# Performance work log

Measured on AMD Instinct MI355X. Metric: run time of the kernel, lower is better.

## Reference

```python
import jax, jax.numpy as jnp
import numpy as np

B, D, T = 32, 1024, 1000
LMAX = 200
VOCAB = 80
BLANK = VOCAB - 1
NEG = -1e30


def setup_inputs() -> dict:
    key = jax.random.key(0)
    ks = jax.random.split(key, 8)
    decoder_outputs = jax.random.normal(ks[0], (B, D, T), dtype=jnp.float32)
    target_text = jax.random.randint(ks[1], (B, LMAX), 0, BLANK, dtype=jnp.int32)
    decoder_lengths = jax.random.randint(ks[2], (B,), T // 2, T + 1, dtype=jnp.int32)
    target_lengths = jax.random.randint(ks[3], (B,), 1, LMAX + 1, dtype=jnp.int32)
    # learned params (dropout is identity in eval / deterministic reference)
    W1 = jax.random.normal(ks[4], (D, D), dtype=jnp.float32) * (1.0 / np.sqrt(D))
    b1 = jnp.zeros((D,), dtype=jnp.float32)
    W2 = jax.random.normal(ks[5], (D, VOCAB), dtype=jnp.float32) * (1.0 / np.sqrt(D))
    b2 = jnp.zeros((VOCAB,), dtype=jnp.float32)
    return {"decoder_outputs": decoder_outputs, "target_text": target_text,
            "decoder_lengths": decoder_lengths, "target_lengths": target_lengths,
            "W1": W1, "b1": b1, "W2": W2, "b2": b2}


def _ctc_nll(log_probs, targets, input_lengths, target_lengths):
    # log_probs: [T, B, V]; standard CTC alpha (forward) DP over extended labels.
    Tt, Bb, V = log_probs.shape
    L = targets.shape[1]
    S = 2 * L + 1
    ext = jnp.full((Bb, S), BLANK, dtype=targets.dtype).at[:, 1::2].set(targets)
    ext_m2 = jnp.pad(ext, ((0, 0), (2, 0)), constant_values=BLANK)[:, :S]
    allow_skip = (ext != BLANK) & (ext != ext_m2)
    allow_skip = allow_skip.at[:, :2].set(False)

    lp0 = log_probs[0]  # [B, V]
    alpha0 = jnp.full((Bb, S), NEG, dtype=log_probs.dtype)
    alpha0 = alpha0.at[:, 0].set(lp0[:, BLANK])
    alpha0 = alpha0.at[:, 1].set(jnp.take_along_axis(lp0, targets[:, :1], axis=1)[:, 0])

    def step(alpha, inp):
        lp_t, t = inp
        emit = jnp.take_along_axis(lp_t, ext, axis=1)  # [B, S]
        a2 = jnp.pad(alpha, ((0, 0), (1, 0)), constant_values=NEG)[:, :S]
        a3 = jnp.pad(alpha, ((0, 0), (2, 0)), constant_values=NEG)[:, :S]
        a3 = jnp.where(allow_skip, a3, NEG)
        new = jnp.logaddexp(jnp.logaddexp(alpha, a2), a3) + emit
        alpha = jnp.where((t < input_lengths)[:, None], new, alpha)
        return alpha, None

    alpha, _ = jax.lax.scan(step, alpha0, (log_probs[1:], jnp.arange(1, Tt)))
    i1 = (2 * target_lengths - 1)[:, None]
    i2 = (2 * target_lengths)[:, None]
    last = jnp.logaddexp(jnp.take_along_axis(alpha, i1, axis=1)[:, 0],
                         jnp.take_along_axis(alpha, i2, axis=1)[:, 0])
    nll = -last
    # zero_infinity=True: invalid alignments -> 0 loss
    return jnp.where(last > NEG / 2, nll, 0.0)


def reference(decoder_outputs, target_text, decoder_lengths, target_lengths, W1, b1, W2, b2):
    x = jnp.transpose(decoder_outputs, (0, 2, 1))          # [B, T, D]
    h = jax.nn.relu(jnp.einsum('btd,de->bte', x, W1) + b1)  # proj + ReLU (dropout=identity)
    logits = jnp.einsum('btd,dv->btv', h, W2) + b2          # [B, T, V]
    log_probs = jax.nn.log_softmax(logits, axis=2)
    log_probs = jnp.transpose(log_probs, (1, 0, 2))         # [T, B, V]
    ctc_loss = _ctc_nll(log_probs, target_text, decoder_lengths, target_lengths)
    return (ctc_loss / decoder_lengths.astype(jnp.float32)).mean()
```

## Files before the change

### kernel.cpp

```cpp
#include <hip/hip_runtime.h>
#include <cstdint>
#include <cstddef>

#define BN_ 32
#define DD_ 1024
#define TT_ 1000
#define LMAX_ 200
#define VC_ 80
#define BLANK_ 79
#define SS_ 401
#define SPAD 512
#define EMW 320
#define NEGV (-1e30f)

typedef _Float16 half8 __attribute__((ext_vector_type(8)));
typedef _Float16 half4 __attribute__((ext_vector_type(4)));
typedef float f32x4 __attribute__((ext_vector_type(4)));

__device__ __forceinline__ void async16(const void* g, void* l) {
  __builtin_amdgcn_global_load_lds(
      (const __attribute__((address_space(1))) unsigned int*)g,
      (__attribute__((address_space(3))) unsigned int*)l, 16, 0, 0);
}

__global__ __launch_bounds__(512) void transpose_all_kernel(
    const float* __restrict__ dec, const float* __restrict__ W1,
    const float* __restrict__ W2, _Float16* __restrict__ Af,
    _Float16* __restrict__ W1T, _Float16* __restrict__ W2T) {
  __shared__ _Float16 T2[64 * 256];
  int z = blockIdx.z;
  const float* in; _Float16* out; int C;
  const int R = 1024;
  if (z < 32) {
    in = dec + (size_t)z * R * TT_;
    out = Af + (size_t)z * TT_ * R;
    C = TT_;
  } else if (z == 32) {
    in = W1; out = W1T; C = 1024;
  } else {
    in = W2; out = W2T; C = VC_;
  }
  int c0 = blockIdx.x * 256, r0 = blockIdx.y * 64;
  if (c0 >= C) return;
  int tid = threadIdx.x;
  int cl = tid & 63, w = tid >> 6;
  int cch = c0 + 4 * cl;
  bool cv = (cch < C);
#pragma unroll
  for (int i = 0; i < 8; ++i) {
    int rl = w * 8 + i;
    f32x4 f = {0.f, 0.f, 0.f, 0.f};
    if (cv) f = *(const f32x4*)(in + (size_t)(r0 + rl) * C + cch);
    half4 hv = {(_Float16)f.x, (_Float16)f.y, (_Float16)f.z, (_Float16)f.w};
    *(half4*)&T2[rl * 256 + 4 * cl] = hv;
  }
  __syncthreads();
  {
    int cr = tid & 255, rh = (tid >> 8) * 32;
    if (c0 + cr < C) {
      half8 ho[4];
#pragma unroll
      for (int k = 0; k < 4; ++k)
#pragma unroll
        for (int j = 0; j < 8; ++j)
          ho[k][j] = T2[(rh + k * 8 + j) * 256 + cr];
      _Float16* op = out + (size_t)(c0 + cr) * R + r0 + rh;
#pragma unroll
      for (int k = 0; k < 4; ++k) *(half8*)&op[k * 8] = ho[k];
    }
  }
}

__device__ __forceinline__ void stage_half(const _Float16* __restrict__ X,
                                           int x0, int kt, int h,
                                           _Float16* lds, int tid, int K) {
#pragma unroll
  for (int jj = 0; jj < 2; ++jj) {
    int seg = tid + 512 * jj;
    int row = seg >> 3, slot = seg & 7;
    int cg = slot ^ (row & 7);
    async16(X + (size_t)(x0 + h * 128 + row) * K + kt * 64 + cg * 8,
            lds + seg * 8);
  }
}

__global__ __launch_bounds__(512, 2) void gemm_relu_kernel(
    const _Float16* __restrict__ A, const _Float16* __restrict__ Bt,
    const float* __restrict__ bias, _Float16* __restrict__ H,
    int M, int N, int K) {
  __shared__ __align__(16) _Float16 sA[2][16384];
  __shared__ __align__(16) _Float16 sB[2][16384];
  int tid = threadIdx.x;
  int wave = tid >> 6, lane = tid & 63;
  int quad = lane >> 4, r16 = lane & 15;
  int wm = wave >> 2, wn = wave & 3;

  int orig = blockIdx.x, nwg = gridDim.x;
  int xcd = orig & 7, loc = orig >> 3;
  int qq = nwg >> 3, rr = nwg & 7;
  int wg = (xcd < rr ? xcd * (qq + 1) : rr * (qq + 1) + (xcd - rr) * qq) + loc;
  int m0 = (wg >> 2) * 256, n0 = (wg & 3) * 256;

  f32x4 acc[4][8];
#pragma unroll
  for (int q = 0; q < 4; ++q)
#pragma unroll
    for (int f = 0; f < 8; ++f) acc[q][f] = {0.f, 0.f, 0.f, 0.f};

  stage_half(A, m0, 0, 0, &sA[0][0], tid, K);
  stage_half(A, m0, 0, 1, &sA[0][8192], tid, K);
  stage_half(Bt, n0, 0, 0, &sB[0][0], tid, K);
  stage_half(Bt, n0, 0, 1, &sB[0][8192], tid, K);
  stage_half(A, m0, 1, 0, &sA[1][0], tid, K);
  stage_half(Bt, n0, 1, 0, &sB[1][0], tid, K);
  stage_half(A, m0, 1, 1, &sA[1][8192], tid, K);
  asm volatile("s_waitcnt vmcnt(6)" ::: "memory");
  __builtin_amdgcn_s_barrier();

  const int NKT = K >> 6;
#pragma unroll 2
  for (int t = 0; t < NKT; ++t) {
    int cur = t & 1, nxt = cur ^ 1;
    int t1 = (t + 1 < NKT) ? t + 1 : NKT - 1;
    int t2 = (t + 2 < NKT) ? t + 2 : NKT - 1;
    const _Float16* As = sA[cur];
    const _Float16* Bs = sB[cur];
    int sw0 = ((0 * 4 + quad) ^ (r16 & 7)) * 8;
    int sw1 = ((1 * 4 + quad) ^ (r16 & 7)) * 8;
    half8 af[4][2];
    half8 bfr[2][2][2];
#pragma unroll
    for (int q = 0; q < 4; ++q) {
      const int qm = q >> 1, qn = q & 1;
      if (qn == 0) {
        int abase = (qm * 128 + wm * 64 + r16) * 64;
#pragma unroll
        for (int i = 0; i < 4; ++i) {
          af[i][0] = *(const half8*)&As[abase + i * 16 * 64 + sw0];
          af[i][1] = *(const half8*)&As[abase + i * 16 * 64 + sw1];
        }
      }
      if (qm == 0) {
        int bbase = (qn * 128 + wn * 32 + r16) * 64;
#pragma unroll
        for (int j = 0; j < 2; ++j) {
          bfr[qn][j][0] = *(const half8*)&Bs[bbase + j * 16 * 64 + sw0];
          bfr[qn][j][1] = *(const half8*)&Bs[bbase + j * 16 * 64 + sw1];
        }
      }
      if (q == 0) stage_half(Bt, n0, t1, 1, &sB[nxt][8192], tid, K);
      else if (q == 1) stage_half(A, m0, t2, 0, &sA[cur][0], tid, K);
      else if (q == 2) stage_half(Bt, n0, t2, 0, &sB[cur][0], tid, K);
      else stage_half(A, m0, t2, 1, &sA[cur][8192], tid, K);
      __builtin_amdgcn_s_barrier();
      asm volatile("s_waitcnt lgkmcnt(0)" ::: "memory");
      __builtin_amdgcn_s_setprio(1);
#pragma unroll
      for (int i = 0; i < 4; ++i)
#pragma unroll
        for (int j = 0; j < 2; ++j) {
          acc[q][i * 2 + j] = __builtin_amdgcn_mfma_f32_16x16x32_f16(
              af[i][0], bfr[qn][j][0], acc[q][i * 2 + j], 0, 0, 0);
          acc[q][i * 2 + j] = __builtin_amdgcn_mfma_f32_16x16x32_f16(
              af[i][1], bfr[qn][j][1], acc[q][i * 2 + j], 0, 0, 0);
        }
      __builtin_amdgcn_s_setprio(0);
      if (q == 3) asm volatile("s_waitcnt vmcnt(6)" ::: "memory");
      __builtin_amdgcn_s_barrier();
    }
  }
  asm volatile("s_waitcnt vmcnt(0)" ::: "memory");

  float bvv[2][2];
#pragma unroll
  for (int qn = 0; qn < 2; ++qn)
#pragma unroll
    for (int j = 0; j < 2; ++j)
      bvv[qn][j] = bias[n0 + qn * 128 + wn * 32 + j * 16 + r16];
#pragma unroll
  for (int q = 0; q < 4; ++q) {
    const int qm = q >> 1, qn = q & 1;
#pragma unroll
    for (int i = 0; i < 4; ++i)
#pragma unroll
      for (int j = 0; j < 2; ++j) {
#pragma unroll
        for (int r = 0; r < 4; ++r) {
          int m = m0 + qm * 128 + wm * 64 + i * 16 + quad * 4 + r;
          int n = n0 + qn * 128 + wn * 32 + j * 16 + r16;
          float v = acc[q][i * 2 + j][r] + bvv[qn][j];
          H[(size_t)m * N + n] = (_Float16)fmaxf(v, 0.f);
        }
      }
  }
}

__global__ __launch_bounds__(256) void gemm_prob_kernel(
    const _Float16* __restrict__ A, const _Float16* __restrict__ Bt,
    const float* __restrict__ bias, const int* __restrict__ targets,
    float* __restrict__ EM, int M, int K) {
  constexpr int BK = 64;
  __shared__ __align__(16) _Float16 sA[64 * BK];
  __shared__ __align__(16) _Float16 sB[VC_ * BK];
  __shared__ float sP[64][VC_];
  int tid = threadIdx.x;
  int wave = tid >> 6, lane = tid & 63;
  int quad = lane >> 4, r16 = lane & 15;
  int m0 = blockIdx.x * 64;

  f32x4 acc[5];
#pragma unroll
  for (int j = 0; j < 5; ++j) acc[j] = {0.f, 0.f, 0.f, 0.f};

  for (int kt = 0; kt < K; kt += BK) {
#pragma unroll
    for (int jj = 0; jj < 2; ++jj) {
      int seg = tid + 256 * jj;
      int row = seg >> 3, slot = seg & 7;
      int cg = slot ^ (row & 7);
      async16(A + (size_t)(m0 + row) * K + kt + cg * 8, &sA[seg * 8]);
    }
#pragma unroll
    for (int jj = 0; jj < 3; ++jj) {
      int seg = tid + 256 * jj;
      if (seg < VC_ * 8) {
        int row = seg >> 3, slot = seg & 7;
        int cg = slot ^ (row & 7);
        async16(Bt + (size_t)row * K + kt + cg * 8, &sB[seg * 8]);
      }
    }
    __syncthreads();
#pragma unroll
    for (int ku = 0; ku < 2; ++ku) {
      int sw = ((ku * 4 + quad) ^ (r16 & 7)) * 8;
      half8 af = *(const half8*)&sA[(wave * 16 + r16) * BK + sw];
      half8 bfr[5];
#pragma unroll
      for (int j = 0; j < 5; ++j)
        bfr[j] = *(const half8*)&sB[(j * 16 + r16) * BK + sw];
#pragma unroll
      for (int j = 0; j < 5; ++j)
        acc[j] = __builtin_amdgcn_mfma_f32_16x16x32_f16(af, bfr[j], acc[j], 0, 0, 0);
    }
    __syncthreads();
  }
  float bv[5];
#pragma unroll
  for (int j = 0; j < 5; ++j) bv[j] = bias[j * 16 + r16];
#pragma unroll
  for (int rr = 0; rr < 4; ++rr) {
    float vals[5];
    float mx = -3.4e38f;
#pragma unroll
    for (int j = 0; j < 5; ++j) {
      vals[j] = acc[j][rr] + bv[j];
      mx = fmaxf(mx, vals[j]);
    }
#pragma unroll
    for (int d = 1; d < 16; d <<= 1) mx = fmaxf(mx, __shfl_xor(mx, d));
    float ex[5], sm = 0.f;
#pragma unroll
    for (int j = 0; j < 5; ++j) { ex[j] = __expf(vals[j] - mx); sm += ex[j]; }
#pragma unroll
    for (int d = 1; d < 16; d <<= 1) sm += __shfl_xor(sm, d);
    float rinv = 1.f / sm;
    int ml = wave * 16 + quad * 4 + rr;
#pragma unroll
    for (int j = 0; j < 5; ++j) sP[ml][j * 16 + r16] = ex[j] * rinv;
  }
  __syncthreads();

  {
    int row = tid >> 2, q4 = tid & 3;
    int m = m0 + row;
    int b = m / TT_;
    const int* tg = targets + b * LMAX_;
    const float* pr = sP[row];
    float pb = pr[BLANK_];
    float* o = EM + (size_t)m * EMW + q4 * 80;
#pragma unroll 4
    for (int sc = 0; sc < 80; sc += 4) {
      int l = q4 * 80 + sc;
      float4 vv;
      vv.x = (l + 0 < LMAX_) ? pr[tg[l + 0]] : ((l + 0 >= 256) ? pb : 0.f);
      vv.y = (l + 1 < LMAX_) ? pr[tg[l + 1]] : ((l + 1 >= 256) ? pb : 0.f);
      vv.z = (l + 2 < LMAX_) ? pr[tg[l + 2]] : ((l + 2 >= 256) ? pb : 0.f);
      vv.w = (l + 3 < LMAX_) ? pr[tg[l + 3]] : ((l + 3 >= 256) ? pb : 0.f);
      *(float4*)o = vv;
      o += 4;
    }
  }
}

__device__ __forceinline__ void dp_step_fwd(float (&bta)[8], int& k,
                                            const f32x4 e0, const f32x4 e1,
                                            const float (&am)[4], int lane) {
  float pm1 = __shfl_up(bta[7], 1);
  int pk = __shfl_up(k, 1);
  if (lane == 0) { pm1 = 0.f; pk = k; }
  int knew = max(k, pk);
  pm1 = ldexpf(pm1, pk - knew);
  int ds = k - knew;
#pragma unroll
  for (int r = 0; r < 8; ++r) bta[r] = ldexpf(bta[r], ds);
  k = knew;
  float nb[8];
  nb[0] = (bta[0] + pm1) * e0.x;
  nb[1] = fmaf(am[0], pm1, bta[1] + bta[0]) * e0.y;
  nb[2] = (bta[2] + bta[1]) * e0.z;
  nb[3] = fmaf(am[1], bta[1], bta[3] + bta[2]) * e0.w;
  nb[4] = (bta[4] + bta[3]) * e1.x;
  nb[5] = fmaf(am[2], bta[3], bta[5] + bta[4]) * e1.y;
  nb[6] = (bta[6] + bta[5]) * e1.z;
  nb[7] = fmaf(am[3], bta[5], bta[7] + bta[6]) * e1.w;
#pragma unroll
  for (int r = 0; r < 8; ++r) bta[r] = nb[r];
}

__device__ __forceinline__ void dp_step_bwd(float (&g)[8], int& k,
                                            const f32x4 e0, const f32x4 e1,
                                            const float (&amB)[4], int lane) {
  float gh[8];
  gh[0] = g[0] * e0.x; gh[1] = g[1] * e0.y;
  gh[2] = g[2] * e0.z; gh[3] = g[3] * e0.w;
  gh[4] = g[4] * e1.x; gh[5] = g[5] * e1.y;
  gh[6] = g[6] * e1.z; gh[7] = g[7] * e1.w;
  float qm1 = __shfl_down(gh[0], 1);
  float qm2 = __shfl_down(gh[1], 1);
  int nk = __shfl_down(k, 1);
  if (lane == 63) { qm1 = 0.f; qm2 = 0.f; nk = k; }
  int knew = max(k, nk);
  int dq = nk - knew;
  qm1 = ldexpf(qm1, dq);
  qm2 = ldexpf(qm2, dq);
  int ds = k - knew;
#pragma unroll
  for (int r = 0; r < 8; ++r) gh[r] = ldexpf(gh[r], ds);
  k = knew;
  g[0] = gh[0] + gh[1];
  g[1] = fmaf(amB[0], gh[3], gh[1] + gh[2]);
  g[2] = gh[2] + gh[3];
  g[3] = fmaf(amB[1], gh[5], gh[3] + gh[4]);
  g[4] = gh[4] + gh[5];
  g[5] = fmaf(amB[2], gh[7], gh[5] + gh[6]);
  g[6] = gh[6] + gh[7];
  g[7] = fmaf(amB[3], qm2, gh[7] + qm1);
}

__device__ __forceinline__ void dp_rescale(float (&v)[8], int& k) {
  float m = fmaxf(fmaxf(fmaxf(v[0], v[1]), fmaxf(v[2], v[3])),
                  fmaxf(fmaxf(v[4], v[5]), fmaxf(v[6], v[7])));
  int ex = (__float_as_int(m) >> 23) - 126;
  k += ex;
#pragma unroll
  for (int r = 0; r < 8; ++r) v[r] = ldexpf(v[r], -ex);
}

__device__ __forceinline__ float allow_f(const int* __restrict__ tg, int s) {
  if (!(s & 1) || s < 3) return 0.f;
  int li = s >> 1;
  if (li >= LMAX_) return 0.f;
  int lab = tg[li];
  return (lab != BLANK_ && lab != tg[li - 1]) ? 1.f : 0.f;
}

__global__ __launch_bounds__(128) void ctc_dp_kernel(
    const float* __restrict__ EM, const int* __restrict__ targets,
    const int* __restrict__ dlen, const int* __restrict__ tlen,
    float* __restrict__ out) {
  __shared__ float sg[SPAD];
  __shared__ int skg[64];
  int b = blockIdx.x;
  int wave = threadIdx.x >> 6;
  int lane = threadIdx.x & 63;
  const float* em4 = EM + (size_t)b * TT_ * EMW + lane * 4;
  const float* embl = EM + (size_t)b * TT_ * EMW + 256 + lane;
  const int* tg = targets + b * LMAX_;
  int Tl = dlen[b], Ll = tlen[b];
  int tm = Tl >> 1;

  constexpr int PD = 8;
  f32x4 pf[PD];
  float pb[PD];
  float v[8];
  int k = 0;

  if (wave == 0) {
    float am[4];
#pragma unroll
    for (int j = 0; j < 4; ++j) am[j] = allow_f(tg, lane * 8 + 2 * j + 1);
    f32x4 lv0 = *(const f32x4*)(em4);
    float bl0 = embl[0];
#pragma unroll
    for (int r = 0; r < 8; ++r) v[r] = 0.f;
    if (lane == 0) { v[0] = bl0; v[1] = lv0.x; }
#pragma unroll
    for (int j = 0; j < PD; ++j) {
      int ri = min(1 + j, TT_ - 1);
      pf[j] = *(const f32x4*)(em4 + (size_t)ri * EMW);
      pb[j] = embl[(size_t)ri * EMW];
    }
    int t = 1;
    for (; t + (PD - 1) <= tm; t += PD) {
#pragma unroll
      for (int u = 0; u < PD; ++u) {
        f32x4 lv = pf[u]; float bl = pb[u];
        f32x4 e0 = {bl, lv.x, bl, lv.y};
        f32x4 e1 = {bl, lv.z, bl, lv.w};
        dp_step_fwd(v, k, e0, e1, am, lane);
        if (u & 1) dp_rescale(v, k);
        int ri = min(t + u + PD, TT_ - 1);
        pf[u] = *(const f32x4*)(em4 + (size_t)ri * EMW);
        pb[u] = embl[(size_t)ri * EMW];
      }
    }
#pragma unroll
    for (int u = 0; u < PD; ++u) {
      if (t + u <= tm) {
        f32x4 lv = pf[u]; float bl = pb[u];
        f32x4 e0 = {bl, lv.x, bl, lv.y};
        f32x4 e1 = {bl, lv.z, bl, lv.w};
        dp_step_fwd(v, k, e0, e1, am, lane);
        if (u & 1) dp_rescale(v, k);
      }
    }
  } else {
    float amB[4];
#pragma unroll
    for (int j = 0; j < 4; ++j) amB[j] = allow_f(tg, lane * 8 + 2 * j + 3);
    int s1 = 2 * Ll - 1, s2 = 2 * Ll;
#pragma unroll
    for (int r = 0; r < 8; ++r) {
      int s = lane * 8 + r;
      v[r] = (s == s1 || s == s2) ? 1.f : 0.f;
    }
#pragma unroll
    for (int j = 0; j < PD; ++j) {
      int ri = max(Tl - 1 - j, 0);
      pf[j] = *(const f32x4*)(em4 + (size_t)ri * EMW);
      pb[j] = embl[(size_t)ri * EMW];
    }
    int t = Tl - 1;
    for (; t - (PD - 1) > tm; t -= PD) {
#pragma unroll
      for (int u = 0; u < PD; ++u) {
        f32x4 lv = pf[u]; float bl = pb[u];
        f32x4 e0 = {bl, lv.x, bl, lv.y};
        f32x4 e1 = {bl, lv.z, bl, lv.w};
        dp_step_bwd(v, k, e0, e1, amB, lane);
        if (u & 1) dp_rescale(v, k);
        int ri = max(t - u - PD, 0);
        pf[u] = *(const f32x4*)(em4 + (size_t)ri * EMW);
        pb[u] = embl[(size_t)ri * EMW];
      }
    }
#pragma unroll
    for (int u = 0; u < PD; ++u) {
      if (t - u > tm) {
        f32x4 lv = pf[u]; float bl = pb[u];
        f32x4 e0 = {bl, lv.x, bl, lv.y};
        f32x4 e1 = {bl, lv.z, bl, lv.w};
        dp_step_bwd(v, k, e0, e1, amB, lane);
        if (u & 1) dp_rescale(v, k);
      }
    }
#pragma unroll
    for (int r = 0; r < 8; ++r) sg[lane * 8 + r] = v[r];
    skg[lane] = k;
  }
  __syncthreads();
  if (wave == 0) {
    float p = 0.f;
#pragma unroll
    for (int r = 0; r < 8; ++r) p = fmaf(v[r], sg[lane * 8 + r], p);
    int kk = k + skg[lane];
    if (p == 0.f) kk = -(1 << 30);
#pragma unroll
    for (int d = 1; d < 64; d <<= 1) {
      float po = __shfl_xor(p, d);
      int ko = __shfl_xor(kk, d);
      int km = max(kk, ko);
      p = ldexpf(p, kk - km) + ldexpf(po, ko - km);
      kk = km;
    }
    if (lane == 0) {
      float nll = 0.f;
      if (p > 0.f) nll = -((log2f(p) + (float)kk) * 0.69314718055994531f);
      atomicAdd(out, nll / (float)Tl * (1.f / BN_));
    }
  }
}

extern "C" void kernel_launch(void* const* d_in, const int* in_sizes, int n_in,
                              void* d_out, int out_size, void* d_ws, size_t ws_size,
                              hipStream_t stream) {
  const float* dec = (const float*)d_in[0];
  const int* tgt   = (const int*)d_in[1];
  const int* dln   = (const int*)d_in[2];
  const int* tln   = (const int*)d_in[3];
  const float* W1  = (const float*)d_in[4];
  const float* b1  = (const float*)d_in[5];
  const float* W2  = (const float*)d_in[6];
  const float* b2  = (const float*)d_in[7];
  float* out = (float*)d_out;

  char* ws = (char*)d_ws;
  const size_t M = (size_t)BN_ * TT_;
  _Float16* Af   = (_Float16*)(ws);
  float* EM      = (float*)(ws);
  _Float16* Hf   = (_Float16*)(ws + 65536000);
  _Float16* W1T  = (_Float16*)(ws + 131072000);
  _Float16* W2T  = (_Float16*)(ws + 133169152);

  hipMemsetAsync(d_out, 0, sizeof(float), stream);

  transpose_all_kernel<<<dim3(4, 16, 34), 512, 0, stream>>>(
      dec, W1, W2, Af, W1T, W2T);
  gemm_relu_kernel<<<dim3((1024 / 256) * (M / 256), 1, 1), 512, 0, stream>>>(
      Af, W1T, b1, Hf, (int)M, DD_, DD_);
  gemm_prob_kernel<<<dim3(M / 64, 1, 1), 256, 0, stream>>>(
      Hf, W2T, b2, tgt, EM, (int)M, DD_);
  ctc_dp_kernel<<<dim3(BN_, 1, 1), 128, 0, stream>>>(EM, tgt, dln, tln, out);
}
```

Baseline: 396.5 us.

## Double-buffer second GEMM loads and swizzle transpose LDS to avoid bank conflicts

The vocab-projection GEMM now uses two LDS stages with async global-to-LDS prefetch two tiles ahead, explicit vmcnt waits and raised MFMA priority, so loads overlap the matrix math instead of stalling at each barrier. The transpose/convert kernel gets an XOR-swizzled LDS layout and a new read mapping that gives 16-byte contiguous global writes. The B-tile loop drops its row guard, so it now reads rows 80..95 of the transposed W2 buffer and relies on that memory being valid. The hand-written waitcnt counts must match the number of issued loads.

```diff
diff --git a/kernel.cpp b/kernel.cpp
--- a/kernel.cpp
+++ b/kernel.cpp
@@ -52,21 +52,28 @@
     f32x4 f = {0.f, 0.f, 0.f, 0.f};
     if (cv) f = *(const f32x4*)(in + (size_t)(r0 + rl) * C + cch);
     half4 hv = {(_Float16)f.x, (_Float16)f.y, (_Float16)f.z, (_Float16)f.w};
-    *(half4*)&T2[rl * 256 + 4 * cl] = hv;
+    int key = ((((rl >> 3) & 7) ^ (cl & 7) ^ ((cl >> 4) & 3)) << 4);
+    int wb = (rl * 512 + 8 * cl) ^ key;
+    *(half4*)((char*)T2 + wb) = hv;
   }
   __syncthreads();
   {
-    int cr = tid & 255, rh = (tid >> 8) * 32;
-    if (c0 + cr < C) {
-      half8 ho[4];
-#pragma unroll
-      for (int k = 0; k < 4; ++k)
-#pragma unroll
-        for (int j = 0; j < 8; ++j)
-          ho[k][j] = T2[(rh + k * 8 + j) * 256 + cr];
-      _Float16* op = out + (size_t)(c0 + cr) * R + r0 + rh;
-#pragma unroll
-      for (int k = 0; k < 4; ++k) *(half8*)&op[k * 8] = ho[k];
+    int t8 = tid & 7, ct = tid >> 3;
+#pragma unroll
+    for (int i = 0; i < 4; ++i) {
+      int cr = ct + i * 64;
+      if (c0 + cr < C) {
+        half8 ho;
+#pragma unroll
+        for (int j = 0; j < 8; ++j) {
+          int r = t8 * 8 + j;
+          int key = ((((r >> 3) & 7) ^ ((cr >> 2) & 7) ^ ((cr >> 6) & 3)) << 4);
+          int rb = (r * 512 + 2 * cr) ^ key;
+          ho[j] = *(const _Float16*)((char*)T2 + rb);
+        }
+        _Float16* op = out + (size_t)(c0 + cr) * R + r0 + t8 * 8;
+        *(half8*)op = ho;
+      }
     }
   }
 }
@@ -200,8 +207,8 @@
     const float* __restrict__ bias, const int* __restrict__ targets,
     float* __restrict__ EM, int M, int K) {
   constexpr int BK = 64;
-  __shared__ __align__(16) _Float16 sA[64 * BK];
-  __shared__ __align__(16) _Float16 sB[VC_ * BK];
+  __shared__ __align__(16) _Float16 sA[2][64 * BK];
+  __shared__ __align__(16) _Float16 sB[2][96 * BK];
   __shared__ float sP[64][VC_];
   int tid = threadIdx.x;
   int wave = tid >> 6, lane = tid & 63;
@@ -212,38 +219,61 @@
 #pragma unroll
   for (int j = 0; j < 5; ++j) acc[j] = {0.f, 0.f, 0.f, 0.f};
 
-  for (int kt = 0; kt < K; kt += BK) {
+  auto stageA = [&](int kt, _Float16* dst) {
 #pragma unroll
     for (int jj = 0; jj < 2; ++jj) {
       int seg = tid + 256 * jj;
       int row = seg >> 3, slot = seg & 7;
       int cg = slot ^ (row & 7);
-      async16(A + (size_t)(m0 + row) * K + kt + cg * 8, &sA[seg * 8]);
-    }
+      async16(A + (size_t)(m0 + row) * K + kt + cg * 8, dst + seg * 8);
+    }
+  };
+  auto stageB = [&](int kt, _Float16* dst) {
 #pragma unroll
     for (int jj = 0; jj < 3; ++jj) {
       int seg = tid + 256 * jj;
-      if (seg < VC_ * 8) {
-        int row = seg >> 3, slot = seg & 7;
-        int cg = slot ^ (row & 7);
-        async16(Bt + (size_t)row * K + kt + cg * 8, &sB[seg * 8]);
-      }
-    }
-    __syncthreads();
+      int row = seg >> 3, slot = seg & 7;
+      int cg = slot ^ (row & 7);
+      async16(Bt + (size_t)row * K + kt + cg * 8, dst + seg * 8);
+    }
+  };
+
+  stageA(0, sA[0]); stageB(0, sB[0]);
+  stageA(BK, sA[1]); stageB(BK, sB[1]);
+  asm volatile("s_waitcnt vmcnt(5)" ::: "memory");
+  __builtin_amdgcn_s_barrier();
+
+  const int NKT = K / BK;
+  for (int t = 0; t < NKT; ++t) {
+    int cur = t & 1;
+    int kt2 = (t + 2 < NKT ? t + 2 : NKT - 1) * BK;
+    const _Float16* As = sA[cur];
+    const _Float16* Bs = sB[cur];
+    half8 af[2], bfr[5][2];
 #pragma unroll
     for (int ku = 0; ku < 2; ++ku) {
       int sw = ((ku * 4 + quad) ^ (r16 & 7)) * 8;
-      half8 af = *(const half8*)&sA[(wave * 16 + r16) * BK + sw];
-      half8 bfr[5];
+      af[ku] = *(const half8*)&As[(wave * 16 + r16) * BK + sw];
 #pragma unroll
       for (int j = 0; j < 5; ++j)
-        bfr[j] = *(const half8*)&sB[(j * 16 + r16) * BK + sw];
+        bfr[j][ku] = *(const half8*)&Bs[(j * 16 + r16) * BK + sw];
+    }
+    asm volatile("s_waitcnt lgkmcnt(0)" ::: "memory");
+    __builtin_amdgcn_s_barrier();
+    stageA(kt2, sA[cur]); stageB(kt2, sB[cur]);
+    __builtin_amdgcn_s_setprio(1);
+#pragma unroll
+    for (int ku = 0; ku < 2; ++ku)
 #pragma unroll
       for (int j = 0; j < 5; ++j)
-        acc[j] = __builtin_amdgcn_mfma_f32_16x16x32_f16(af, bfr[j], acc[j], 0, 0, 0);
-    }
-    __syncthreads();
-  }
+        acc[j] = __builtin_amdgcn_mfma_f32_16x16x32_f16(
+            af[ku], bfr[j][ku], acc[j], 0, 0, 0);
+    __builtin_amdgcn_s_setprio(0);
+    asm volatile("s_waitcnt vmcnt(5)" ::: "memory");
+    __builtin_amdgcn_s_barrier();
+  }
+  asm volatile("s_waitcnt vmcnt(0)" ::: "memory");
+
   float bv[5];
 #pragma unroll
   for (int j = 0; j < 5; ++j) bv[j] = bias[j * 16 + r16];
```

After: 396.8 us. No clear change (+0.1%).
